# Kernel tuning notes

Measured on AMD Instinct MI355X. Metric: run time of the kernel, lower is better.

## Reference

```python
import jax, jax.numpy as jnp
import numpy as np

K = 3          # kernel_size
CV = 256       # vision_dim
WD = 768       # word_dim
B = 16         # batch
NC = 128       # number of classes / words
OUT_DIM = CV * K * K + 1


def setup_inputs() -> dict:
    key = jax.random.key(0)
    ks = jax.random.split(key, 18)
    n = lambda k, s, sc=1.0: jax.random.normal(k, s, jnp.float32) * sc
    u = lambda k, s: jax.random.uniform(k, s, jnp.float32, 0.5, 1.5)
    return {
        "x": n(ks[0], (B, 2 * CV, 24, 24)),
        "word": n(ks[1], (NC, B, WD)),
        # vis[1]: conv_layer(512, 512, 3, pad=1) -> Conv2d(no bias) + BN
        "conv1_w": n(ks[2], (2 * CV, 2 * CV, 3, 3), 0.02),
        "bn1_g": u(ks[3], (2 * CV,)),
        "bn1_b": n(ks[4], (2 * CV,), 0.1),
        "bn1_m": n(ks[5], (2 * CV,), 0.1),
        "bn1_v": u(ks[6], (2 * CV,)),
        # vis[3]: conv_layer(512, 256, 3, pad=1)
        "conv2_w": n(ks[7], (CV, 2 * CV, 3, 3), 0.02),
        "bn2_g": u(ks[8], (CV,)),
        "bn2_b": n(ks[9], (CV,), 0.1),
        "bn2_m": n(ks[10], (CV,), 0.1),
        "bn2_v": u(ks[11], (CV,)),
        # vis[4]: Conv2d(256, 256, 1) with bias
        "conv3_w": n(ks[12], (CV, CV, 1, 1), 0.05),
        "conv3_b": n(ks[13], (CV,), 0.05),
        # txt: Linear(word_dim, C*K*K + 1)
        "txt_w": n(ks[14], (OUT_DIM, WD), 0.02),
        "txt_b": n(ks[15], (OUT_DIM,), 0.02),
    }


def _up2(x):
    # nn.Upsample(scale_factor=2, mode='bilinear', align_corners=False)
    b, c, h, w = x.shape
    return jax.image.resize(x, (b, c, 2 * h, 2 * w), method="bilinear")


def _conv(x, w, pad):
    return jax.lax.conv_general_dilated(
        x, w, (1, 1), [(pad, pad), (pad, pad)],
        dimension_numbers=("NCHW", "OIHW", "NCHW"))


def _bn(x, g, b, m, v):
    # BatchNorm2d in inference form (running stats), eps=1e-5
    inv = g * jax.lax.rsqrt(v + 1e-5)
    return x * inv[None, :, None, None] + (b - m * inv)[None, :, None, None]


def _forward(x, word, conv1_w, bn1_g, bn1_b, bn1_m, bn1_v,
             conv2_w, bn2_g, bn2_b, bn2_m, bn2_v,
             conv3_w, conv3_b, txt_w, txt_b):
    # vis backbone: up2 -> conv3x3/BN/ReLU -> up2 -> conv3x3/BN/ReLU -> conv1x1
    v = jax.nn.relu(_bn(_conv(_up2(x), conv1_w, 1), bn1_g, bn1_b, bn1_m, bn1_v))
    v = jax.nn.relu(_bn(_conv(_up2(v), conv2_w, 1), bn2_g, bn2_b, bn2_m, bn2_v))
    v = _conv(v, conv3_w, 0) + conv3_b[None, :, None, None]   # (B, C, H, W)
    b, c, h, w = v.shape
    nc = word.shape[0]
    # text -> per-(word, image) conv filters and biases
    t = word @ txt_w.T + txt_b                 # (Nc, B, C*K*K + 1)
    wk = t[..., :-1].reshape(nc, b, c, K, K)   # (Nc, B, C, K, K)
    bias = t[..., -1]                          # (Nc, B)
    # batched dynamic conv as one grouped conv: group g = image g
    rhs = jnp.transpose(wk, (1, 0, 2, 3, 4)).reshape(b * nc, c, K, K)
    lhs = v.reshape(1, b * c, h, w)
    out = jax.lax.conv_general_dilated(
        lhs, rhs, (1, 1), [(K // 2, K // 2)] * 2,
        dimension_numbers=("NCHW", "OIHW", "NCHW"), feature_group_count=b)
    out = out.reshape(b, nc, h, w) + bias.T[:, :, None, None]
    return out  # (B, Nc, H, W)


def reference(x, word, conv1_w, bn1_g, bn1_b, bn1_m, bn1_v,
              conv2_w, bn2_g, bn2_b, bn2_m, bn2_v,
              conv3_w, conv3_b, txt_w, txt_b):
    return _forward(x, word, conv1_w, bn1_g, bn1_b, bn1_m, bn1_v,
                    conv2_w, bn2_g, bn2_b, bn2_m, bn2_v,
                    conv3_w, conv3_b, txt_w, txt_b)
```

## Files before the change

### kernel.cpp

```cpp
#include <hip/hip_runtime.h>
#include <cstdint>
#include <cstddef>

typedef unsigned short ushort_t;
typedef short bf16x8 __attribute__((ext_vector_type(8)));
typedef float f32x4 __attribute__((ext_vector_type(4)));

__device__ __forceinline__ float bf2f(ushort_t h) {
  union { unsigned u; float f; } v; v.u = ((unsigned)h) << 16; return v.f;
}
__device__ __forceinline__ ushort_t f2bf(float f) {
  union { float f; unsigned u; } v; v.f = f;
  unsigned u = v.u;
  return (ushort_t)((u + 0x7fffu + ((u >> 16) & 1u)) >> 16);
}

#define GLOAD16(g, l)                                                         \
  __builtin_amdgcn_global_load_lds(                                           \
      (const __attribute__((address_space(1))) void*)(g),                     \
      (__attribute__((address_space(3))) void*)(l), 16, 0, 0)

__global__ __launch_bounds__(256) void wprep(const float* __restrict__ in,
                                             ushort_t* __restrict__ out,
                                             int CO, int C, int KS2) {
  int idx = blockIdx.x * 256 + threadIdx.x;
  int total = CO * C * KS2;
  if (idx >= total) return;
  int co  = idx / (C * KS2);
  int rem = idx - co * (C * KS2);
  int tap = rem / C;
  int c   = rem - tap * C;
  out[idx] = f2bf(in[(size_t)co * C * KS2 + (size_t)c * KS2 + tap]);
}

__global__ __launch_bounds__(256) void fsplit(const float* __restrict__ in,
                                              ushort_t* __restrict__ hi,
                                              ushort_t* __restrict__ lo,
                                              int rows_in, long long total) {
  long long idx = (long long)blockIdx.x * 256 + threadIdx.x;
  if (idx >= total) return;
  long long r = idx / 768;
  float x = (r < rows_in) ? in[idx] : 0.f;
  ushort_t h = f2bf(x);
  hi[idx] = h;
  lo[idx] = f2bf(x - bf2f(h));
}

__global__ __launch_bounds__(256) void border_zero(ushort_t* __restrict__ buf,
                                                   int B, int PH, int PW, int C) {
  int nb = 2 * PW + 2 * (PH - 2);
  long long total = (long long)B * nb * C;
  long long idx = (long long)blockIdx.x * 256 + threadIdx.x;
  if (idx >= total) return;
  int c = (int)(idx % C);
  long long r = idx / C;
  int bp = (int)(r % nb);
  int b = (int)(r / nb);
  int y, x;
  if (bp < PW) { y = 0; x = bp; }
  else if (bp < 2 * PW) { y = PH - 1; x = bp - PW; }
  else { int e = bp - 2 * PW; y = 1 + (e >> 1); x = (e & 1) ? PW - 1 : 0; }
  buf[((size_t)(b * PH + y) * PW + x) * C + c] = 0;
}

__global__ __launch_bounds__(256) void upsample1(const float* __restrict__ in,
                                                 ushort_t* __restrict__ out) {
  int idx = blockIdx.x * 256 + threadIdx.x;
  if (idx >= 16 * 48 * 48 * 512) return;
  int c = idx & 511;
  int px = idx >> 9;
  int x = px % 48; int rest = px / 48; int y = rest % 48; int b = rest / 48;
  int jy = y >> 1, jx = x >> 1;
  int y0, y1, x0, x1; float wy0, wy1, wx0, wx1;
  if (y & 1) { y0 = jy; y1 = (jy + 1 < 24) ? jy + 1 : 23; wy0 = 0.75f; wy1 = 0.25f; }
  else       { y0 = (jy > 0) ? jy - 1 : 0; y1 = jy; wy0 = 0.25f; wy1 = 0.75f; }
  if (x & 1) { x0 = jx; x1 = (jx + 1 < 24) ? jx + 1 : 23; wx0 = 0.75f; wx1 = 0.25f; }
  else       { x0 = (jx > 0) ? jx - 1 : 0; x1 = jx; wx0 = 0.25f; wx1 = 0.75f; }
  const float* p = in + ((size_t)b * 512 + c) * 576;
  float v = wy0 * (wx0 * p[y0 * 24 + x0] + wx1 * p[y0 * 24 + x1]) +
            wy1 * (wx0 * p[y1 * 24 + x0] + wx1 * p[y1 * 24 + x1]);
  out[(((size_t)b * 50 + y + 1) * 50 + (x + 1)) * 512 + c] = f2bf(v);
}

__global__ __launch_bounds__(256) void upsample2(const ushort_t* __restrict__ in,
                                                 ushort_t* __restrict__ out) {
  int idx = blockIdx.x * 256 + threadIdx.x;
  if (idx >= 16 * 96 * 96 * 512) return;
  int c = idx & 511;
  int px = idx >> 9;
  int x = px % 96; int rest = px / 96; int y = rest % 96; int b = rest / 96;
  int jy = y >> 1, jx = x >> 1;
  int y0, y1, x0, x1; float wy0, wy1, wx0, wx1;
  if (y & 1) { y0 = jy; y1 = (jy + 1 < 48) ? jy + 1 : 47; wy0 = 0.75f; wy1 = 0.25f; }
  else       { y0 = (jy > 0) ? jy - 1 : 0; y1 = jy; wy0 = 0.25f; wy1 = 0.75f; }
  if (x & 1) { x0 = jx; x1 = (jx + 1 < 48) ? jx + 1 : 47; wx0 = 0.75f; wx1 = 0.25f; }
  else       { x0 = (jx > 0) ? jx - 1 : 0; x1 = jx; wx0 = 0.25f; wx1 = 0.75f; }
  const ushort_t* p = in + (size_t)b * 48 * 48 * 512 + c;
  float v = wy0 * (wx0 * bf2f(p[(y0 * 48 + x0) * 512]) + wx1 * bf2f(p[(y0 * 48 + x1) * 512])) +
            wy1 * (wx0 * bf2f(p[(y1 * 48 + x0) * 512]) + wx1 * bf2f(p[(y1 * 48 + x1) * 512]));
  out[(((size_t)b * 98 + y + 1) * 98 + (x + 1)) * 512 + c] = f2bf(v);
}

__global__ __launch_bounds__(256, 2) void text_mfma(
    const ushort_t* __restrict__ wh, const ushort_t* __restrict__ wl,
    const ushort_t* __restrict__ th, const ushort_t* __restrict__ tl,
    const float* __restrict__ tb,
    ushort_t* __restrict__ wkbuf, float* __restrict__ dynbias) {
  __shared__ ushort_t Ahs[128 * 64];
  __shared__ ushort_t Als[128 * 64];
  __shared__ ushort_t Bhs[128 * 64];
  __shared__ ushort_t Bls[128 * 64];
  const int tid = threadIdx.x;
  const int lane = tid & 63;
  const int wid = tid >> 6;
  const int n0 = blockIdx.x * 128;
  const int m0 = blockIdx.y * 128;
  const int soff = ((lane & 7) ^ ((lane >> 3) & 7)) * 16;
  const int g8 = lane >> 3;
  const char *pah[4], *pal[4], *pbh[4], *pbl[4];
#pragma unroll
  for (int j = 0; j < 4; ++j) {
    int row = wid * 32 + j * 8 + g8;
    size_t ab = (size_t)(m0 + row) * 1536 + soff;
    pah[j] = (const char*)wh + ab;
    pal[j] = (const char*)wl + ab;
    size_t bb = (size_t)(n0 + row) * 1536 + soff;
    pbh[j] = (const char*)th + bb;
    pbl[j] = (const char*)tl + bb;
  }
  const int lr = lane & 15, hi4 = lane >> 4;
  const int cow = (wid >> 1) * 64;
  const int pxw = (wid & 1) * 64;
  int aoff[4], boff[4];
#pragma unroll
  for (int r = 0; r < 4; ++r) {
    int row = cow + r * 16 + lr;
    aoff[r] = row * 128 + ((hi4 ^ (row & 7)) * 16);
    row = pxw + r * 16 + lr;
    boff[r] = row * 128 + ((hi4 ^ (row & 7)) * 16);
  }
  f32x4 acc[4][4];
#pragma unroll
  for (int r = 0; r < 4; ++r)
#pragma unroll
    for (int q = 0; q < 4; ++q) acc[r][q] = (f32x4){0.f, 0.f, 0.f, 0.f};

#pragma unroll 1
  for (int k0 = 0; k0 < 768; k0 += 64) {
    const int kb = k0 * 2;
#pragma unroll
    for (int j = 0; j < 4; ++j) {
      const int ld = (wid * 4 + j) * 1024;
      GLOAD16(pah[j] + kb, (char*)Ahs + ld);
      GLOAD16(pal[j] + kb, (char*)Als + ld);
      GLOAD16(pbh[j] + kb, (char*)Bhs + ld);
      GLOAD16(pbl[j] + kb, (char*)Bls + ld);
    }
    __syncthreads();
#pragma unroll
    for (int ks = 0; ks < 2; ++ks) {
      const int kx = ks * 64;
      bf16x8 ah[4], al[4], bh[4], bl[4];
#pragma unroll
      for (int r = 0; r < 4; ++r) {
        ah[r] = *(const bf16x8*)((const char*)Ahs + (aoff[r] ^ kx));
        al[r] = *(const bf16x8*)((const char*)Als + (aoff[r] ^ kx));
        bh[r] = *(const bf16x8*)((const char*)Bhs + (boff[r] ^ kx));
        bl[r] = *(const bf16x8*)((const char*)Bls + (boff[r] ^ kx));
      }
#pragma unroll
      for (int r = 0; r < 4; ++r)
#pragma unroll
        for (int q = 0; q < 4; ++q)
          acc[r][q] = __builtin_amdgcn_mfma_f32_16x16x32_bf16(ah[r], bh[q], acc[r][q], 0, 0, 0);
#pragma unroll
      for (int r = 0; r < 4; ++r)
#pragma unroll
        for (int q = 0; q < 4; ++q)
          acc[r][q] = __builtin_amdgcn_mfma_f32_16x16x32_bf16(ah[r], bl[q], acc[r][q], 0, 0, 0);
#pragma unroll
      for (int r = 0; r < 4; ++r)
#pragma unroll
        for (int q = 0; q < 4; ++q)
          acc[r][q] = __builtin_amdgcn_mfma_f32_16x16x32_bf16(al[r], bh[q], acc[r][q], 0, 0, 0);
    }
    __syncthreads();
  }

#pragma unroll
  for (int r = 0; r < 4; ++r) {
#pragma unroll
    for (int q = 0; q < 4; ++q) {
      int n = n0 + pxw + q * 16 + lr;
      if (n > 2304) continue;
      float tbn = tb[n];
#pragma unroll
      for (int j = 0; j < 4; ++j) {
        int m = m0 + cow + r * 16 + hi4 * 4 + j;
        float v = acc[r][q][j] + tbn;
        if (n < 2304) {
          int c = n / 9, tap = n - c * 9;
          int nc = m >> 4, bb = m & 15;
          wkbuf[((size_t)bb * 128 + nc) * 2304 + tap * 256 + c] = f2bf(v);
        } else {
          dynbias[m] = v;
        }
      }
    }
  }
}

template <int KS, int EPI, int BM, int BN, int MW, int NW, int H, int W, int C,
          int MOUT, bool PIW, bool OPAD>
__global__ __launch_bounds__(256, 2) void conv_mfma(
    const ushort_t* __restrict__ in, const ushort_t* __restrict__ wt,
    const float* __restrict__ p0, const float* __restrict__ p1,
    const float* __restrict__ p2, const float* __restrict__ p3,
    ushort_t* __restrict__ outb, float* __restrict__ outf) {
  constexpr int WAVES = 4;
  constexpr int AINST = BM / (8 * WAVES);
  constexpr int BINST = BN / (8 * WAVES);
  constexpr int MR = BM / MW / 16;
  constexpr int NR = BN / NW / 16;
  constexpr int KK = KS * KS;
  constexpr int PHI = (KS == 3) ? H + 2 : H;
  constexpr int PWI = (KS == 3) ? W + 2 : W;
  __shared__ ushort_t Asm[BM * 64];
  __shared__ ushort_t Bsm[BN * 64];

  const int tid = threadIdx.x;
  const int lane = tid & 63;
  const int wid = tid >> 6;
  const int p0t = blockIdx.x * BN;
  const int co0 = blockIdx.y * BM;
  const int b = blockIdx.z;

  const int soff = ((lane & 7) ^ ((lane >> 3) & 7)) * 16;

  const char* wbase = (const char*)wt + (PIW ? (size_t)b * MOUT * KK * C * 2 : 0);
  const char* aptr[AINST];
#pragma unroll
  for (int j = 0; j < AINST; ++j) {
    int arow = wid * (AINST * 8) + j * 8 + (lane >> 3);
    aptr[j] = wbase + (size_t)(co0 + arow) * ((size_t)KK * C * 2) + soff;
  }
  const char* ibase = (const char*)in + (size_t)b * PHI * PWI * C * 2;
  const char* bptr[BINST];
#pragma unroll
  for (int i = 0; i < BINST; ++i) {
    int brow = wid * (BINST * 8) + i * 8 + (lane >> 3);
    int p = p0t + brow;
    int y = p / W, x = p % W;
    int off = (KS == 3) ? ((y + 1) * PWI + (x + 1)) : (y * W + x);
    bptr[i] = ibase + (size_t)off * C * 2 + soff;
  }

  const int lr = lane & 15, hi = lane >> 4;
  const int cow = (wid / NW) * (BM / MW);
  const int pxw = (wid % NW) * (BN / NW);
  int aoff[MR], boff[NR];
#pragma unroll
  for (int r = 0; r < MR; ++r) {
    int row = cow + r * 16 + lr;
    aoff[r] = row * 128 + ((hi ^ (row & 7)) * 16);
  }
#pragma unroll
  for (int q = 0; q < NR; ++q) {
    int row = pxw + q * 16 + lr;
    boff[q] = row * 128 + ((hi ^ (row & 7)) * 16);
  }

  f32x4 acc[MR][NR];
#pragma unroll
  for (int r = 0; r < MR; ++r)
#pragma unroll
    for (int q = 0; q < NR; ++q) acc[r][q] = (f32x4){0.f, 0.f, 0.f, 0.f};

#pragma unroll 1
  for (int tap = 0; tap < KK; ++tap) {
    const int toff = (KS == 3) ? ((tap / 3 - 1) * PWI + (tap % 3 - 1)) * C * 2 : 0;
#pragma unroll 1
    for (int c0 = 0; c0 < C; c0 += 64) {
      const int koff = (tap * C + c0) * 2;
#pragma unroll
      for (int j = 0; j < AINST; ++j)
        GLOAD16(aptr[j] + koff, (char*)Asm + (wid * AINST + j) * 1024);
#pragma unroll
      for (int i = 0; i < BINST; ++i)
        GLOAD16(bptr[i] + toff + c0 * 2, (char*)Bsm + (wid * BINST + i) * 1024);
      __syncthreads();
#pragma unroll
      for (int ks = 0; ks < 2; ++ks) {
        const int kx = ks * 64;
        bf16x8 af[MR], bfv[NR];
#pragma unroll
        for (int r = 0; r < MR; ++r)
          af[r] = *(const bf16x8*)((const char*)Asm + (aoff[r] ^ kx));
#pragma unroll
        for (int q = 0; q < NR; ++q)
          bfv[q] = *(const bf16x8*)((const char*)Bsm + (boff[q] ^ kx));
#pragma unroll
        for (int r = 0; r < MR; ++r)
#pragma unroll
          for (int q = 0; q < NR; ++q)
            acc[r][q] = __builtin_amdgcn_mfma_f32_16x16x32_bf16(af[r], bfv[q], acc[r][q], 0, 0, 0);
      }
      __syncthreads();
    }
  }

#pragma unroll
  for (int r = 0; r < MR; ++r) {
    const int co = co0 + cow + r * 16 + hi * 4;
    float sc[4], sh[4];
#pragma unroll
    for (int j = 0; j < 4; ++j) {
      if (EPI == 0) {
        float inv = p0[co + j] * rsqrtf(p3[co + j] + 1e-5f);
        sc[j] = inv; sh[j] = p1[co + j] - p2[co + j] * inv;
      } else if (EPI == 1) {
        sc[j] = 1.f; sh[j] = p0[co + j];
      }
    }
#pragma unroll
    for (int q = 0; q < NR; ++q) {
      int p = p0t + pxw + q * 16 + lr;
      int y = p / W, x = p % W;
      if (EPI == 2) {
#pragma unroll
        for (int j = 0; j < 4; ++j) {
          float v = acc[r][q][j] + p0[(co + j) * 16 + b];
          outf[(((size_t)b * MOUT + co + j) * H + y) * W + x] = v;
        }
      } else {
        ushort_t pk[4];
#pragma unroll
        for (int j = 0; j < 4; ++j) {
          float v = acc[r][q][j] * sc[j] + sh[j];
          if (EPI == 0) v = fmaxf(v, 0.f);
          pk[j] = f2bf(v);
        }
        size_t oidx = OPAD
            ? (((size_t)b * (H + 2) + y + 1) * (W + 2) + x + 1) * MOUT + co
            : (((size_t)b * H + y) * W + x) * MOUT + co;
        *(uint2*)&outb[oidx] = *(const uint2*)pk;
      }
    }
  }
}

__global__ __launch_bounds__(256) void fill_zero(float* __restrict__ p, int n) {
  int i = blockIdx.x * 256 + threadIdx.x;
  if (i < n) p[i] = 0.f;
}

extern "C" void kernel_launch(void* const* d_in, const int* in_sizes, int n_in,
                              void* d_out, int out_size, void* d_ws, size_t ws_size,
                              hipStream_t stream) {
  (void)in_sizes; (void)n_in;
  const float* x       = (const float*)d_in[0];
  const float* word    = (const float*)d_in[1];
  const float* conv1_w = (const float*)d_in[2];
  const float* bn1_g   = (const float*)d_in[3];
  const float* bn1_b   = (const float*)d_in[4];
  const float* bn1_m   = (const float*)d_in[5];
  const float* bn1_v   = (const float*)d_in[6];
  const float* conv2_w = (const float*)d_in[7];
  const float* bn2_g   = (const float*)d_in[8];
  const float* bn2_b   = (const float*)d_in[9];
  const float* bn2_m   = (const float*)d_in[10];
  const float* bn2_v   = (const float*)d_in[11];
  const float* conv3_w = (const float*)d_in[12];
  const float* conv3_b = (const float*)d_in[13];
  const float* txt_w   = (const float*)d_in[14];
  const float* txt_b   = (const float*)d_in[15];
  float* out = (float*)d_out;

  char* ws = (char*)d_ws;
  size_t off = 0;
  auto alloc = [&](size_t bytes) -> void* {
    void* p = ws + off;
    off += bytes;
    off = (off + 255) & ~(size_t)255;
    return p;
  };
  ushort_t* P0  = (ushort_t*)alloc((size_t)16 * 98 * 98 * 512 * 2);
  ushort_t* up1 = P0;
  ushort_t* up2 = P0;
  ushort_t* vb  = P0;
  ushort_t* a1  = (ushort_t*)alloc((size_t)16 * 48 * 48 * 512 * 2);
  ushort_t* w1b = (ushort_t*)alloc((size_t)512 * 4608 * 2);
  ushort_t* w2b = (ushort_t*)alloc((size_t)256 * 4608 * 2);
  ushort_t* w3b = (ushort_t*)alloc((size_t)256 * 256 * 2);
  ushort_t* wkb = (ushort_t*)alloc((size_t)16 * 128 * 2304 * 2);
  float*    dyb = (float*)alloc((size_t)2048 * 4);
  ushort_t* whi = (ushort_t*)alloc((size_t)2048 * 768 * 2);
  ushort_t* wlo = (ushort_t*)alloc((size_t)2048 * 768 * 2);
  ushort_t* twh = (ushort_t*)alloc((size_t)2432 * 768 * 2);
  ushort_t* twl = (ushort_t*)alloc((size_t)2432 * 768 * 2);
  ushort_t* a2  = (ushort_t*)d_out;

  if (ws_size < off) {
    fill_zero<<<(out_size + 255) / 256, 256, 0, stream>>>(out, out_size);
    return;
  }

  wprep<<<(512 * 4608 + 255) / 256, 256, 0, stream>>>(conv1_w, w1b, 512, 512, 9);
  wprep<<<(256 * 4608 + 255) / 256, 256, 0, stream>>>(conv2_w, w2b, 256, 512, 9);
  wprep<<<(256 * 256 + 255) / 256, 256, 0, stream>>>(conv3_w, w3b, 256, 256, 1);
  {
    long long nw = (long long)2048 * 768;
    fsplit<<<(int)((nw + 255) / 256), 256, 0, stream>>>(word, whi, wlo, 2048, nw);
    long long nt = (long long)2432 * 768;
    fsplit<<<(int)((nt + 255) / 256), 256, 0, stream>>>(txt_w, twh, twl, 2305, nt);
  }
  text_mfma<<<dim3(19, 16), 256, 0, stream>>>(whi, wlo, twh, twl, txt_b, wkb, dyb);

  {
    long long nbz = (long long)16 * (2 * 50 + 2 * 48) * 512;
    border_zero<<<(int)((nbz + 255) / 256), 256, 0, stream>>>(up1, 16, 50, 50, 512);
    int n = 16 * 48 * 48 * 512;
    upsample1<<<(n + 255) / 256, 256, 0, stream>>>(x, up1);
  }
  conv_mfma<3, 0, 256, 128, 2, 2, 48, 48, 512, 512, false, false>
      <<<dim3(18, 2, 16), 256, 0, stream>>>(up1, w1b, bn1_g, bn1_b, bn1_m, bn1_v,
                                            a1, nullptr);
  {
    long long nbz = (long long)16 * (2 * 98 + 2 * 96) * 512;
    border_zero<<<(int)((nbz + 255) / 256), 256, 0, stream>>>(up2, 16, 98, 98, 512);
    int n = 16 * 96 * 96 * 512;
    upsample2<<<(n + 255) / 256, 256, 0, stream>>>(a1, up2);
  }
  conv_mfma<3, 0, 256, 128, 2, 2, 96, 96, 512, 256, false, false>
      <<<dim3(72, 1, 16), 256, 0, stream>>>(up2, w2b, bn2_g, bn2_b, bn2_m, bn2_v,
                                            a2, nullptr);
  {
    long long nbz = (long long)16 * (2 * 98 + 2 * 96) * 256;
    border_zero<<<(int)((nbz + 255) / 256), 256, 0, stream>>>(vb, 16, 98, 98, 256);
  }
  conv_mfma<1, 1, 256, 128, 2, 2, 96, 96, 256, 256, false, true>
      <<<dim3(72, 1, 16), 256, 0, stream>>>(a2, w3b, conv3_b, nullptr, nullptr, nullptr,
                                            vb, nullptr);
  conv_mfma<3, 2, 128, 256, 1, 4, 96, 96, 256, 128, true, false>
      <<<dim3(36, 1, 16), 256, 0, stream>>>(vb, wkb, dyb, nullptr, nullptr, nullptr,
                                            nullptr, out);
}
```

Measured before the change: 1.282 ms.

## Add 8-wave 256x256-tile conv kernel with interleaved loads and MFMA phases

Adds a new implicit-GEMM conv kernel that uses 512 threads and 256x256 output tiles for the two 3x3 conv+BN+ReLU layers. Each K step is split into four MFMA phases, with global-to-LDS loads for the next stage spread between them, plus barriers and s_setprio around the MFMA bursts. The larger tile raises reuse per byte loaded and the interleaving is meant to overlap memory traffic with matrix math. In exchange, register and LDS pressure go up (128KB LDS per block), occupancy may drop, and the grid has fewer blocks.

```diff
diff --git a/kernel.cpp b/kernel.cpp
--- a/kernel.cpp
+++ b/kernel.cpp
@@ -206,6 +206,177 @@
           dynbias[m] = v;
         }
       }
+    }
+  }
+}
+
+template <int H, int W, int C, int MOUT>
+__global__ __launch_bounds__(512, 2) void conv_mfma8(
+    const ushort_t* __restrict__ in, const ushort_t* __restrict__ wt,
+    const float* __restrict__ gg, const float* __restrict__ bb2,
+    const float* __restrict__ mm, const float* __restrict__ vv,
+    ushort_t* __restrict__ outb) {
+  constexpr int PHI = H + 2, PWI = W + 2;
+  constexpr int CC = C / 64;
+  constexpr int NT = 9 * CC;
+  __shared__ ushort_t lds[2 * 512 * 64];
+
+  const int tid = threadIdx.x;
+  const int lane = tid & 63;
+  const int wid = tid >> 6;
+  const int p0t = blockIdx.x * 256;
+  const int co0 = blockIdx.y * 256;
+  const int b = blockIdx.z;
+
+  const int soff = ((tid & 7) ^ ((tid >> 3) & 7)) * 16;
+  const int rowi = tid >> 3;
+
+  const char* aptr[4];
+#pragma unroll
+  for (int j = 0; j < 4; ++j)
+    aptr[j] = (const char*)wt + (size_t)(co0 + j * 64 + rowi) * ((size_t)9 * C * 2) + soff;
+  const char* ibase = (const char*)in + (size_t)b * PHI * PWI * C * 2;
+  const char* bptr[4];
+#pragma unroll
+  for (int i = 0; i < 4; ++i) {
+    int p = p0t + i * 64 + rowi;
+    int y = p / W, x = p % W;
+    bptr[i] = ibase + (size_t)((y + 1) * PWI + (x + 1)) * C * 2 + soff;
+  }
+
+  const int lr = lane & 15, hi = lane >> 4;
+  const int cow = (wid >> 2) * 128;
+  const int pxw = (wid & 3) * 64;
+  int aoff[8], boff[4];
+#pragma unroll
+  for (int r = 0; r < 8; ++r) {
+    int row = cow + r * 16 + lr;
+    aoff[r] = row * 128 + ((hi ^ (row & 7)) * 16);
+  }
+#pragma unroll
+  for (int q = 0; q < 4; ++q) {
+    int row = pxw + q * 16 + lr;
+    boff[q] = 32768 + row * 128 + ((hi ^ (row & 7)) * 16);
+  }
+
+  f32x4 acc[8][4];
+#pragma unroll
+  for (int r = 0; r < 8; ++r)
+#pragma unroll
+    for (int q = 0; q < 4; ++q) acc[r][q] = (f32x4){0.f, 0.f, 0.f, 0.f};
+
+  auto dec = [&](int t, int& ka, int& kb) {
+    int tap = t / CC;
+    int cb = (t - tap * CC) * 128;
+    ka = tap * C * 2 + cb;
+    kb = ((tap / 3 - 1) * PWI + (tap % 3) - 1) * (C * 2) + cb;
+  };
+
+  {
+    int ka, kb; dec(0, ka, kb);
+    char* lb = (char*)lds;
+#pragma unroll
+    for (int j = 0; j < 4; ++j) GLOAD16(aptr[j] + ka, lb + j * 8192 + wid * 1024);
+#pragma unroll
+    for (int i = 0; i < 4; ++i) GLOAD16(bptr[i] + kb, lb + 32768 + i * 8192 + wid * 1024);
+  }
+  asm volatile("s_waitcnt vmcnt(0)" ::: "memory");
+  __builtin_amdgcn_s_barrier();
+
+#pragma unroll 1
+  for (int t = 0; t < NT; ++t) {
+    const char* rb = (const char*)lds + (t & 1) * 65536;
+    char* lb = (char*)lds + ((t & 1) ^ 1) * 65536;
+    int ka = 0, kb = 0;
+    const bool st = (t + 1) < NT;
+    if (st) dec(t + 1, ka, kb);
+
+    bf16x8 af[4], bfv[4];
+    if (st) {
+      GLOAD16(aptr[0] + ka, lb + 0 * 8192 + wid * 1024);
+      GLOAD16(aptr[1] + ka, lb + 1 * 8192 + wid * 1024);
+      GLOAD16(bptr[0] + kb, lb + 32768 + 0 * 8192 + wid * 1024);
+    }
+#pragma unroll
+    for (int q = 0; q < 4; ++q) bfv[q] = *(const bf16x8*)(rb + boff[q]);
+#pragma unroll
+    for (int r = 0; r < 4; ++r) af[r] = *(const bf16x8*)(rb + aoff[r]);
+    __builtin_amdgcn_s_barrier();
+    __builtin_amdgcn_s_setprio(1);
+#pragma unroll
+    for (int r = 0; r < 4; ++r)
+#pragma unroll
+      for (int q = 0; q < 4; ++q)
+        acc[r][q] = __builtin_amdgcn_mfma_f32_16x16x32_bf16(af[r], bfv[q], acc[r][q], 0, 0, 0);
+    __builtin_amdgcn_s_setprio(0);
+    __builtin_amdgcn_s_barrier();
+    if (st) {
+      GLOAD16(aptr[2] + ka, lb + 2 * 8192 + wid * 1024);
+      GLOAD16(aptr[3] + ka, lb + 3 * 8192 + wid * 1024);
+      GLOAD16(bptr[1] + kb, lb + 32768 + 1 * 8192 + wid * 1024);
+    }
+#pragma unroll
+    for (int r = 0; r < 4; ++r) af[r] = *(const bf16x8*)(rb + aoff[r + 4]);
+    __builtin_amdgcn_s_barrier();
+    __builtin_amdgcn_s_setprio(1);
+#pragma unroll
+    for (int r = 0; r < 4; ++r)
+#pragma unroll
+      for (int q = 0; q < 4; ++q)
+        acc[r + 4][q] = __builtin_amdgcn_mfma_f32_16x16x32_bf16(af[r], bfv[q], acc[r + 4][q], 0, 0, 0);
+    __builtin_amdgcn_s_setprio(0);
+    __builtin_amdgcn_s_barrier();
+    if (st) {
+      GLOAD16(bptr[2] + kb, lb + 32768 + 2 * 8192 + wid * 1024);
+      GLOAD16(bptr[3] + kb, lb + 32768 + 3 * 8192 + wid * 1024);
+    }
+#pragma unroll
+    for (int q = 0; q < 4; ++q) bfv[q] = *(const bf16x8*)(rb + (boff[q] ^ 64));
+#pragma unroll
+    for (int r = 0; r < 4; ++r) af[r] = *(const bf16x8*)(rb + (aoff[r] ^ 64));
+    __builtin_amdgcn_s_barrier();
+    __builtin_amdgcn_s_setprio(1);
+#pragma unroll
+    for (int r = 0; r < 4; ++r)
+#pragma unroll
+      for (int q = 0; q < 4; ++q)
+        acc[r][q] = __builtin_amdgcn_mfma_f32_16x16x32_bf16(af[r], bfv[q], acc[r][q], 0, 0, 0);
+    __builtin_amdgcn_s_setprio(0);
+    __builtin_amdgcn_s_barrier();
+#pragma unroll
+    for (int r = 0; r < 4; ++r) af[r] = *(const bf16x8*)(rb + (aoff[r + 4] ^ 64));
+    __builtin_amdgcn_s_barrier();
+    __builtin_amdgcn_s_setprio(1);
+#pragma unroll
+    for (int r = 0; r < 4; ++r)
+#pragma unroll
+      for (int q = 0; q < 4; ++q)
+        acc[r + 4][q] = __builtin_amdgcn_mfma_f32_16x16x32_bf16(af[r], bfv[q], acc[r + 4][q], 0, 0, 0);
+    __builtin_amdgcn_s_setprio(0);
+    asm volatile("s_waitcnt vmcnt(0)" ::: "memory");
+    __builtin_amdgcn_s_barrier();
+  }
+
+#pragma unroll
+  for (int r = 0; r < 8; ++r) {
+    const int co = co0 + cow + r * 16 + hi * 4;
+    float sc[4], sh[4];
+#pragma unroll
+    for (int j = 0; j < 4; ++j) {
+      float inv = gg[co + j] * rsqrtf(vv[co + j] + 1e-5f);
+      sc[j] = inv; sh[j] = bb2[co + j] - mm[co + j] * inv;
+    }
+#pragma unroll
+    for (int q = 0; q < 4; ++q) {
+      int p = p0t + pxw + q * 16 + lr;
+      int y = p / W, x = p % W;
+      ushort_t pk[4];
+#pragma unroll
+      for (int j = 0; j < 4; ++j) {
+        float v = fmaxf(acc[r][q][j] * sc[j] + sh[j], 0.f);
+        pk[j] = f2bf(v);
+      }
+      *(uint2*)&outb[(((size_t)b * H + y) * W + x) * MOUT + co] = *(const uint2*)pk;
     }
   }
 }
@@ -422,18 +593,16 @@
     int n = 16 * 48 * 48 * 512;
     upsample1<<<(n + 255) / 256, 256, 0, stream>>>(x, up1);
   }
-  conv_mfma<3, 0, 256, 128, 2, 2, 48, 48, 512, 512, false, false>
-      <<<dim3(18, 2, 16), 256, 0, stream>>>(up1, w1b, bn1_g, bn1_b, bn1_m, bn1_v,
-                                            a1, nullptr);
+  conv_mfma8<48, 48, 512, 512>
+      <<<dim3(9, 2, 16), 512, 0, stream>>>(up1, w1b, bn1_g, bn1_b, bn1_m, bn1_v, a1);
   {
     long long nbz = (long long)16 * (2 * 98 + 2 * 96) * 512;
     border_zero<<<(int)((nbz + 255) / 256), 256, 0, stream>>>(up2, 16, 98, 98, 512);
     int n = 16 * 96 * 96 * 512;
     upsample2<<<(n + 255) / 256, 256, 0, stream>>>(a1, up2);
   }
-  conv_mfma<3, 0, 256, 128, 2, 2, 96, 96, 512, 256, false, false>
-      <<<dim3(72, 1, 16), 256, 0, stream>>>(up2, w2b, bn2_g, bn2_b, bn2_m, bn2_v,
-                                            a2, nullptr);
+  conv_mfma8<96, 96, 512, 256>
+      <<<dim3(36, 1, 16), 512, 0, stream>>>(up2, w2b, bn2_g, bn2_b, bn2_m, bn2_v, a2);
   {
     long long nbz = (long long)16 * (2 * 98 + 2 * 96) * 256;
     border_zero<<<(int)((nbz + 255) / 256), 256, 0, stream>>>(vb, 16, 98, 98, 256);
```

Measured after the change: 1.298 ms. No clear change (+1.2%).

## Add 512-thread 4-stage pipelined implicit-GEMM conv kernel for the two 3x3 convs

Applied to the files above, without the earlier changes.

Adds a new conv_pipe kernel with 256x256 output tiles, 8 waves, and a 4-deep LDS ring buffer. It streams weight and input K-slices through global_load_lds and controls overlap with explicit vmcnt waits, XOR-swizzled LDS addressing, and raised priority around the MFMA block. BN and ReLU are fused into the epilogue. The two large 3x3 convolutions now use this kernel, with the aim of hiding memory latency and increasing data reuse per tile. In exchange, register pressure is high (128 accumulator floats per thread), the grid is smaller, and each K step needs two barriers.

```diff
diff --git a/kernel.cpp b/kernel.cpp
--- a/kernel.cpp
+++ b/kernel.cpp
@@ -206,6 +206,142 @@
           dynbias[m] = v;
         }
       }
+    }
+  }
+}
+
+template <int H, int W, int C, int MOUT>
+__global__ __launch_bounds__(512, 2) void conv_pipe(
+    const ushort_t* __restrict__ in, const ushort_t* __restrict__ wt,
+    const float* __restrict__ gg, const float* __restrict__ bb2,
+    const float* __restrict__ mm, const float* __restrict__ vv,
+    ushort_t* __restrict__ outb) {
+  constexpr int PHI = H + 2, PWI = W + 2;
+  constexpr int CC = C / 32;
+  constexpr int NT = 9 * CC;
+  __shared__ ushort_t lds[4 * 16384];
+
+  const int tid = threadIdx.x;
+  const int lane = tid & 63;
+  const int wid = tid >> 6;
+  const int p0t = blockIdx.x * 256;
+  const int co0 = blockIdx.y * 256;
+  const int b = blockIdx.z;
+
+  const int soff = ((lane & 3) ^ ((lane >> 3) & 3)) * 16;
+  const int rsub = lane >> 2;
+
+  const char *aptr0, *aptr1, *bptr0, *bptr1;
+  {
+    int r0 = co0 + (wid * 2 + 0) * 16 + rsub;
+    int r1 = co0 + (wid * 2 + 1) * 16 + rsub;
+    aptr0 = (const char*)wt + (size_t)r0 * ((size_t)9 * C * 2) + soff;
+    aptr1 = (const char*)wt + (size_t)r1 * ((size_t)9 * C * 2) + soff;
+    const char* ibase = (const char*)in + (size_t)b * PHI * PWI * C * 2;
+    int pp0 = p0t + (wid * 2 + 0) * 16 + rsub;
+    int pp1 = p0t + (wid * 2 + 1) * 16 + rsub;
+    int y0 = pp0 / W, x0 = pp0 % W;
+    int y1 = pp1 / W, x1 = pp1 % W;
+    bptr0 = ibase + (size_t)((y0 + 1) * PWI + (x0 + 1)) * C * 2 + soff;
+    bptr1 = ibase + (size_t)((y1 + 1) * PWI + (x1 + 1)) * C * 2 + soff;
+  }
+
+  const int lr = lane & 15, hi = lane >> 4;
+  const int cow = (wid >> 2) * 128;
+  const int pxw = (wid & 3) * 64;
+  int aoff[8], boff[4];
+#pragma unroll
+  for (int r = 0; r < 8; ++r) {
+    int ro = cow + r * 16 + lr;
+    aoff[r] = ro * 64 + ((hi ^ ((ro >> 1) & 3)) << 4);
+  }
+#pragma unroll
+  for (int q = 0; q < 4; ++q) {
+    int ro = pxw + q * 16 + lr;
+    boff[q] = 16384 + ro * 64 + ((hi ^ ((ro >> 1) & 3)) << 4);
+  }
+
+  f32x4 acc[8][4];
+#pragma unroll
+  for (int r = 0; r < 8; ++r)
+#pragma unroll
+    for (int q = 0; q < 4; ++q) acc[r][q] = (f32x4){0.f, 0.f, 0.f, 0.f};
+
+  auto stage = [&](int u, int t) {
+    int tap = t / CC;
+    int cb = (t - tap * CC) * 64;
+    int ka = tap * (C * 2) + cb;
+    int kb = ((tap / 3 - 1) * PWI + (tap % 3) - 1) * (C * 2) + cb;
+    char* lb = (char*)lds + u * 32768;
+    GLOAD16(aptr0 + ka, lb + wid * 2048);
+    GLOAD16(aptr1 + ka, lb + wid * 2048 + 1024);
+    GLOAD16(bptr0 + kb, lb + 16384 + wid * 2048);
+    GLOAD16(bptr1 + kb, lb + 16384 + wid * 2048 + 1024);
+  };
+
+  auto compute = [&](int u) {
+    const char* rb = (const char*)lds + u * 32768;
+    bf16x8 af[8], bfv[4];
+#pragma unroll
+    for (int q = 0; q < 4; ++q) bfv[q] = *(const bf16x8*)(rb + boff[q]);
+#pragma unroll
+    for (int r = 0; r < 8; ++r) af[r] = *(const bf16x8*)(rb + aoff[r]);
+    __builtin_amdgcn_s_setprio(1);
+#pragma unroll
+    for (int r = 0; r < 8; ++r)
+#pragma unroll
+      for (int q = 0; q < 4; ++q)
+        acc[r][q] = __builtin_amdgcn_mfma_f32_16x16x32_bf16(af[r], bfv[q], acc[r][q], 0, 0, 0);
+    __builtin_amdgcn_s_setprio(0);
+    __builtin_amdgcn_sched_barrier(0);
+  };
+
+  stage(0, 0); stage(1, 1); stage(2, 2);
+
+#pragma unroll 1
+  for (int t = 0; t < NT - 3; ++t) {
+    stage((t + 3) & 3, t + 3);
+    asm volatile("s_waitcnt vmcnt(12)" ::: "memory");
+    __builtin_amdgcn_s_barrier();
+    __builtin_amdgcn_sched_barrier(0);
+    compute(t & 3);
+    __builtin_amdgcn_s_barrier();
+  }
+  asm volatile("s_waitcnt vmcnt(8)" ::: "memory");
+  __builtin_amdgcn_s_barrier();
+  __builtin_amdgcn_sched_barrier(0);
+  compute((NT - 3) & 3);
+  __builtin_amdgcn_s_barrier();
+  asm volatile("s_waitcnt vmcnt(4)" ::: "memory");
+  __builtin_amdgcn_s_barrier();
+  __builtin_amdgcn_sched_barrier(0);
+  compute((NT - 2) & 3);
+  __builtin_amdgcn_s_barrier();
+  asm volatile("s_waitcnt vmcnt(0)" ::: "memory");
+  __builtin_amdgcn_s_barrier();
+  __builtin_amdgcn_sched_barrier(0);
+  compute((NT - 1) & 3);
+
+#pragma unroll
+  for (int r = 0; r < 8; ++r) {
+    const int co = co0 + cow + r * 16 + hi * 4;
+    float sc[4], sh[4];
+#pragma unroll
+    for (int j = 0; j < 4; ++j) {
+      float inv = gg[co + j] * rsqrtf(vv[co + j] + 1e-5f);
+      sc[j] = inv; sh[j] = bb2[co + j] - mm[co + j] * inv;
+    }
+#pragma unroll
+    for (int q = 0; q < 4; ++q) {
+      int p = p0t + pxw + q * 16 + lr;
+      int y = p / W, x = p % W;
+      ushort_t pk[4];
+#pragma unroll
+      for (int j = 0; j < 4; ++j) {
+        float v = fmaxf(acc[r][q][j] * sc[j] + sh[j], 0.f);
+        pk[j] = f2bf(v);
+      }
+      *(uint2*)&outb[(((size_t)b * H + y) * W + x) * MOUT + co] = *(const uint2*)pk;
     }
   }
 }
@@ -422,18 +558,16 @@
     int n = 16 * 48 * 48 * 512;
     upsample1<<<(n + 255) / 256, 256, 0, stream>>>(x, up1);
   }
-  conv_mfma<3, 0, 256, 128, 2, 2, 48, 48, 512, 512, false, false>
-      <<<dim3(18, 2, 16), 256, 0, stream>>>(up1, w1b, bn1_g, bn1_b, bn1_m, bn1_v,
-                                            a1, nullptr);
+  conv_pipe<48, 48, 512, 512>
+      <<<dim3(9, 2, 16), 512, 0, stream>>>(up1, w1b, bn1_g, bn1_b, bn1_m, bn1_v, a1);
   {
     long long nbz = (long long)16 * (2 * 98 + 2 * 96) * 512;
     border_zero<<<(int)((nbz + 255) / 256), 256, 0, stream>>>(up2, 16, 98, 98, 512);
     int n = 16 * 96 * 96 * 512;
     upsample2<<<(n + 255) / 256, 256, 0, stream>>>(a1, up2);
   }
-  conv_mfma<3, 0, 256, 128, 2, 2, 96, 96, 512, 256, false, false>
-      <<<dim3(72, 1, 16), 256, 0, stream>>>(up2, w2b, bn2_g, bn2_b, bn2_m, bn2_v,
-                                            a2, nullptr);
+  conv_pipe<96, 96, 512, 256>
+      <<<dim3(36, 1, 16), 512, 0, stream>>>(up2, w2b, bn2_g, bn2_b, bn2_m, bn2_v, a2);
   {
     long long nbz = (long long)16 * (2 * 98 + 2 * 96) * 256;
     border_zero<<<(int)((nbz + 255) / 256), 256, 0, stream>>>(vb, 16, 98, 98, 256);
```

Measured after the change: 1.337 ms. +4.3%, slower.
